# Kernel optimization log

Hardware: AMD Instinct MI355X
Metric: run time of the kernel (lower is better)

The kernel has to match this reference:

```python
import jax, jax.numpy as jnp
import numpy as np

N = 8192        # num nodes
D = 512         # hidden_dim
E = 262144      # num edges (avg degree 32)
STEPS = 3       # diffusion_steps


def setup_inputs() -> dict:
    key = jax.random.key(0)
    k1, k2, k3 = jax.random.split(key, 3)
    x = jax.random.normal(k1, (N, D), dtype=jnp.float32)
    edge_index = jax.random.randint(k2, (2, E), 0, N, dtype=jnp.int32)
    W = jax.random.normal(k3, (D, D), dtype=jnp.float32) / np.sqrt(D)
    b = jnp.zeros((D,), dtype=jnp.float32)
    diffusion_weights = jnp.ones((STEPS + 1,), dtype=jnp.float32) / (STEPS + 1)
    return {"x": x, "edge_index": edge_index, "W": W, "b": b,
            "diffusion_weights": diffusion_weights}


def reference(x, edge_index, W, b, diffusion_weights):
    # linear transform
    h = x @ W + b                                   # [N, D]
    # build symmetric normalized dense adjacency (faithful to original)
    row, col = edge_index[0], edge_index[1]
    adj = jnp.zeros((N, N), dtype=h.dtype)
    adj = adj.at[row, col].set(1.0)                 # adj[row, col] = 1
    adj = adj.at[col, row].set(1.0)                 # adj[col, row] = 1
    adj = adj + jnp.eye(N, dtype=h.dtype)           # self loops
    row_sum = adj.sum(axis=1, keepdims=True)
    adj = adj / jnp.maximum(row_sum, 1.0)           # row-normalize, clamp(min=1)
    # K-hop diffusion with learned per-hop weights
    out = diffusion_weights[0] * h
    cur = h
    for i in range(STEPS):
        cur = adj @ cur                             # [N, D]
        out = out + diffusion_weights[i + 1] * cur
    # relu; dropout is identity in eval mode
    return jax.nn.relu(out)
```

## Files before the change

kernel.cpp:

```cpp
#include <hip/hip_runtime.h>
#include <hip/hip_bf16.h>

#define NN 8192
#define DD 512
#define ROWWORDS (NN / 32)
#define MAXDEG 128
#define QCHUNK 256
#define SCL 8.0f

typedef __attribute__((ext_vector_type(8))) short short8;
typedef __attribute__((ext_vector_type(4))) float floatx4;
typedef __attribute__((ext_vector_type(2))) float f32x2;
typedef __attribute__((address_space(1))) const unsigned GASu;
typedef __attribute__((address_space(3))) unsigned LASu;

__device__ __forceinline__ unsigned short f2bf(float f) {
    union { float f; unsigned u; } v; v.f = f;
    unsigned u = v.u;
    return (unsigned short)((u + 0x7FFFu + ((u >> 16) & 1u)) >> 16);
}
__device__ __forceinline__ float bf2f(unsigned short s) {
    union { unsigned x; float f; } v; v.x = (unsigned)s << 16; return v.f;
}

__global__ __launch_bounds__(256) void prep_k(uint4* __restrict__ bm16,
                                              const float* __restrict__ x,
                                              unsigned short* __restrict__ xb,
                                              unsigned char* __restrict__ xq,
                                              const float* __restrict__ W,
                                              unsigned short* __restrict__ wbT,
                                              unsigned char* __restrict__ b1q,
                                              unsigned char* __restrict__ b2q) {
    const int j = blockIdx.x * 256 + threadIdx.x;
    bm16[j] = make_uint4(0u, 0u, 0u, 0u);
    const float4* xv = (const float4*)x;
    float4 v0 = xv[2 * j];
    float4 v1 = xv[2 * j + 1];
    ushort4 o0, o1;
    o0.x = f2bf(v0.x); o0.y = f2bf(v0.y); o0.z = f2bf(v0.z); o0.w = f2bf(v0.w);
    o1.x = f2bf(v1.x); o1.y = f2bf(v1.y); o1.z = f2bf(v1.z); o1.w = f2bf(v1.w);
    ((ushort4*)xb)[2 * j] = o0;
    ((ushort4*)xb)[2 * j + 1] = o1;
    unsigned qa = __builtin_amdgcn_cvt_pk_fp8_f32(SCL * v0.x, SCL * v0.y, 0, false);
    qa = __builtin_amdgcn_cvt_pk_fp8_f32(SCL * v0.z, SCL * v0.w, qa, true);
    unsigned qb = __builtin_amdgcn_cvt_pk_fp8_f32(SCL * v1.x, SCL * v1.y, 0, false);
    qb = __builtin_amdgcn_cvt_pk_fp8_f32(SCL * v1.z, SCL * v1.w, qb, true);
    ((uint2*)xq)[j] = make_uint2(qa, qb);
    if (j < DD * DD / 2) {
#pragma unroll
        for (int r = 0; r < 2; ++r) {
            int idx = j + r * (DD * DD / 2);
            int k = idx >> 9, c = idx & 511;
            wbT[(size_t)c * DD + k] = f2bf(W[idx]);
        }
    }
    if (blockIdx.x < 3 && threadIdx.x < 128) {
        unsigned char* pr = (blockIdx.x == 0 ? xq : blockIdx.x == 1 ? b1q : b2q)
                            + (size_t)NN * DD;
        ((unsigned*)pr)[threadIdx.x] = 0u;
    }
}

__global__ __launch_bounds__(256) void edges_k(const int* __restrict__ ei,
                                               unsigned* __restrict__ bm, int E) {
    int e = blockIdx.x * 256 + threadIdx.x;
    if (e >= E) return;
    int r = ei[e];
    int c = ei[E + e];
    atomicOr(&bm[(size_t)r * ROWWORDS + (c >> 5)], 1u << (c & 31));
    atomicOr(&bm[(size_t)c * ROWWORDS + (r >> 5)], 1u << (r & 31));
}

__global__ __launch_bounds__(256) void decode_k(const unsigned* __restrict__ bm,
                                                unsigned short* __restrict__ cols,
                                                int* __restrict__ deg) {
    const int i = blockIdx.x * 4 + (threadIdx.x >> 6);
    const int t = threadIdx.x & 63;
    const unsigned* rw = bm + (size_t)i * ROWWORDS + t * 4;
    unsigned w0 = rw[0], w1 = rw[1], w2 = rw[2], w3 = rw[3];
    int c = __popc(w0) + __popc(w1) + __popc(w2) + __popc(w3);
    int s = c;
    for (int d = 1; d < 64; d <<= 1) {
        int v = __shfl_up(s, d, 64);
        if (t >= d) s += v;
    }
    int p = s - c;
    const int n = __shfl(s, 63, 64);
    unsigned short* base = cols + (size_t)i * MAXDEG;
    const int cb = t * 128;
#pragma unroll
    for (int q = 0; q < 4; ++q) {
        unsigned w = (q == 0) ? w0 : (q == 1) ? w1 : (q == 2) ? w2 : w3;
        while (w) {
            int b = __ffs(w) - 1;
            w &= (w - 1);
            if (p < MAXDEG) base[p] = (unsigned short)(cb + q * 32 + b);
            ++p;
        }
    }
    if (t == 63) {
        int nc = (n < MAXDEG) ? n : MAXDEG;
        int npad = (nc + 15) & ~15;
        for (int q = nc; q < npad; ++q) base[q] = (unsigned short)NN;
        deg[i] = n;
    }
}

#define CVT(u, w) __builtin_amdgcn_cvt_pk_f32_fp8((int)(u), w)

#define ISSUE(P, js) do { \
    P##0 = *(const unsigned*)(cur + (size_t)(unsigned short)(js)[0] * DD + off); \
    P##1 = *(const unsigned*)(cur + (size_t)(unsigned short)(js)[1] * DD + off); \
    P##2 = *(const unsigned*)(cur + (size_t)(unsigned short)(js)[2] * DD + off); \
    P##3 = *(const unsigned*)(cur + (size_t)(unsigned short)(js)[3] * DD + off); \
    P##4 = *(const unsigned*)(cur + (size_t)(unsigned short)(js)[4] * DD + off); \
    P##5 = *(const unsigned*)(cur + (size_t)(unsigned short)(js)[5] * DD + off); \
    P##6 = *(const unsigned*)(cur + (size_t)(unsigned short)(js)[6] * DD + off); \
    P##7 = *(const unsigned*)(cur + (size_t)(unsigned short)(js)[7] * DD + off); \
} while (0)

#define CONSUME(P) do { \
    lA += CVT(P##0, false); hA += CVT(P##0, true); \
    lB += CVT(P##1, false); hB += CVT(P##1, true); \
    lA += CVT(P##2, false); hA += CVT(P##2, true); \
    lB += CVT(P##3, false); hB += CVT(P##3, true); \
    lA += CVT(P##4, false); hA += CVT(P##4, true); \
    lB += CVT(P##5, false); hB += CVT(P##5, true); \
    lA += CVT(P##6, false); hA += CVT(P##6, true); \
    lB += CVT(P##7, false); hB += CVT(P##7, true); \
} while (0)

__global__ __launch_bounds__(64, 8) void spmm_k(const unsigned char* __restrict__ cur,
                                             unsigned char* __restrict__ nxt,
                                             const unsigned short* __restrict__ cols,
                                             const int* __restrict__ deg,
                                             const float* __restrict__ dw,
                                             const unsigned short* __restrict__ xb,
                                             const unsigned char* __restrict__ b1q,
                                             const unsigned char* __restrict__ b2q,
                                             unsigned short* __restrict__ yb,
                                             int last) {
    const int bid = blockIdx.x;
    const int chunk = bid & 1;
    const int i = bid >> 1;
    const int t = threadIdx.x;
    const int off = chunk * QCHUNK + 4 * t;
    const size_t rowb = (size_t)i * DD;
    const int n = deg[i];
    const int nc = (n < MAXDEG) ? n : MAXDEG;
    const int nb = ((nc + 15) & ~15) >> 3;
    const unsigned short* cl = cols + (size_t)i * MAXDEG;

    const unsigned eu = *(const unsigned*)(cur + rowb + off);

    f32x2 lA = {0.f, 0.f}, hA = lA, lB = lA, hB = lA;
    if (nb) {
        unsigned cA0, cA1, cA2, cA3, cA4, cA5, cA6, cA7;
        unsigned cB0, cB1, cB2, cB3, cB4, cB5, cB6, cB7;
        short8 jsA = *(const short8*)(cl);
        ISSUE(cA, jsA);
        short8 jsB = *(const short8*)(cl + 8);
        ISSUE(cB, jsB);
        for (int b = 2; b < nb; b += 2) {
            short8 jsC = *(const short8*)(cl + (size_t)b * 8);
            short8 jsD = *(const short8*)(cl + (size_t)b * 8 + 8);
            CONSUME(cA);
            ISSUE(cA, jsC);
            CONSUME(cB);
            ISSUE(cB, jsD);
        }
        CONSUME(cA);
        CONSUME(cB);
    }
    f32x2 lo = lA + lB;
    f32x2 hi = hA + hB;
    lo += CVT(eu, false);
    hi += CVT(eu, true);
    const float inv = 1.0f / (float)(n + 1);
    lo *= inv; hi *= inv;

    if (!last) {
        unsigned o = __builtin_amdgcn_cvt_pk_fp8_f32(lo.x, lo.y, 0, false);
        o = __builtin_amdgcn_cvt_pk_fp8_f32(hi.x, hi.y, o, true);
        *(unsigned*)(nxt + rowb + off) = o;
    } else {
        const float w0 = dw[0];
        const float s1 = dw[1] * (1.0f / SCL);
        const float s2 = dw[2] * (1.0f / SCL);
        const float s3 = dw[3] * (1.0f / SCL);
        ushort4 xv = *(const ushort4*)(xb + rowb + off);
        unsigned u1 = *(const unsigned*)(b1q + rowb + off);
        unsigned u2 = *(const unsigned*)(b2q + rowb + off);
        f32x2 b1l = CVT(u1, false), b1h = CVT(u1, true);
        f32x2 b2l = CVT(u2, false), b2h = CVT(u2, true);
        float y0 = w0 * bf2f(xv.x) + s1 * b1l.x + s2 * b2l.x + s3 * lo.x;
        float y1 = w0 * bf2f(xv.y) + s1 * b1l.y + s2 * b2l.y + s3 * lo.y;
        float y2 = w0 * bf2f(xv.z) + s1 * b1h.x + s2 * b2h.x + s3 * hi.x;
        float y3 = w0 * bf2f(xv.w) + s1 * b1h.y + s2 * b2h.y + s3 * hi.y;
        ushort4 o;
        o.x = f2bf(y0); o.y = f2bf(y1); o.z = f2bf(y2); o.w = f2bf(y3);
        *(ushort4*)(yb + rowb + off) = o;
    }
}

__global__ __launch_bounds__(256) void gemm_k(const unsigned short* __restrict__ yb,
                                              const unsigned short* __restrict__ wbT,
                                              const float* __restrict__ bias,
                                              const float* __restrict__ dw, int nw,
                                              float* __restrict__ out) {
    __shared__ unsigned short Asm[128 * 64];
    __shared__ unsigned short Bsm[128 * 64];
    const int t = threadIdx.x;
    const int l = t & 63;
    const int wid = t >> 6;
    const int wm = wid >> 1, wn = wid & 1;
    const int row0 = blockIdx.x * 128;
    const int col0 = blockIdx.y * 128;
    const int lr = l & 15;

    floatx4 acc[4][4];
#pragma unroll
    for (int a = 0; a < 4; ++a)
#pragma unroll
        for (int b = 0; b < 4; ++b) acc[a][b] = (floatx4){0.f, 0.f, 0.f, 0.f};

    for (int k0 = 0; k0 < DD; k0 += 64) {
#pragma unroll
        for (int p = 0; p < 4; ++p) {
            int e = p * 256 + t;
            int r = e >> 3;
            int sl = e & 7;
            int gs = (sl ^ (r & 7)) * 8;
            __builtin_amdgcn_global_load_lds(
                (GASu*)(yb + (size_t)(row0 + r) * DD + k0 + gs),
                (LASu*)(Asm + (size_t)e * 8), 16, 0, 0);
            __builtin_amdgcn_global_load_lds(
                (GASu*)(wbT + (size_t)(col0 + r) * DD + k0 + gs),
                (LASu*)(Bsm + (size_t)e * 8), 16, 0, 0);
        }
        __syncthreads();
#pragma unroll
        for (int ks = 0; ks < 2; ++ks) {
            short8 af[4], bf[4];
#pragma unroll
            for (int mt = 0; mt < 4; ++mt) {
                int R = wm * 64 + mt * 16 + lr;
                int sl = (l >> 4) + 4 * ks;
                af[mt] = *(const short8*)(Asm + R * 64 + (sl ^ (R & 7)) * 8);
            }
#pragma unroll
            for (int nt = 0; nt < 4; ++nt) {
                int R = wn * 64 + nt * 16 + lr;
                int sl = (l >> 4) + 4 * ks;
                bf[nt] = *(const short8*)(Bsm + R * 64 + (sl ^ (R & 7)) * 8);
            }
#pragma unroll
            for (int mt = 0; mt < 4; ++mt)
#pragma unroll
                for (int nt = 0; nt < 4; ++nt)
                    acc[mt][nt] = __builtin_amdgcn_mfma_f32_16x16x32_bf16(
                        af[mt], bf[nt], acc[mt][nt], 0, 0, 0);
        }
        __syncthreads();
    }

    float sb = 0.f;
    for (int q = 0; q < nw; ++q) sb += dw[q];
#pragma unroll
    for (int nt = 0; nt < 4; ++nt) {
        int col = col0 + wn * 64 + nt * 16 + lr;
        float bv = bias[col] * sb;
#pragma unroll
        for (int mt = 0; mt < 4; ++mt) {
            int rowb = row0 + wm * 64 + mt * 16 + (l >> 4) * 4;
#pragma unroll
            for (int r = 0; r < 4; ++r) {
                float v = acc[mt][nt][r] + bv;
                v = fmaxf(v, 0.0f);
                out[(size_t)(rowb + r) * DD + col] = v;
            }
        }
    }
}

extern "C" void kernel_launch(void* const* d_in, const int* in_sizes, int n_in,
                              void* d_out, int out_size, void* d_ws, size_t ws_size,
                              hipStream_t stream) {
    const float* x    = (const float*)d_in[0];
    const int*   ei   = (const int*)d_in[1];
    const float* W    = (const float*)d_in[2];
    const float* bias = (const float*)d_in[3];
    const float* dw   = (const float*)d_in[4];
    const int E = in_sizes[1] / 2;
    const int nw = in_sizes[4];

    char* outc = (char*)d_out;
    unsigned* bitmap     = (unsigned*)outc;
    unsigned short* cols = (unsigned short*)(outc + (size_t)8 * 1024 * 1024);
    int* deg             = (int*)(outc + (size_t)12 * 1024 * 1024);

    const size_t MB = 1024 * 1024;
    char* ws = (char*)d_ws;
    unsigned short* xb  = (unsigned short*)(ws);
    unsigned short* yb  = (unsigned short*)(ws + 8 * MB);
    unsigned short* wbT = (unsigned short*)(ws + 16 * MB);
    unsigned char*  xq  = (unsigned char*)(ws + 17 * MB);
    unsigned char*  b1q = (unsigned char*)(ws + 22 * MB);
    unsigned char*  b2q = (unsigned char*)(ws + 27 * MB);

    prep_k<<<2048, 256, 0, stream>>>((uint4*)bitmap, x, xb, xq, W, wbT, b1q, b2q);
    edges_k<<<(E + 255) / 256, 256, 0, stream>>>(ei, bitmap, E);
    decode_k<<<NN / 4, 256, 0, stream>>>(bitmap, cols, deg);

    spmm_k<<<NN * 2, 64, 0, stream>>>(xq,  b1q, cols, deg, dw, xb, b1q, b2q, yb, 0);
    spmm_k<<<NN * 2, 64, 0, stream>>>(b1q, b2q, cols, deg, dw, xb, b1q, b2q, yb, 0);
    spmm_k<<<NN * 2, 64, 0, stream>>>(b2q, b1q, cols, deg, dw, xb, b1q, b2q, yb, 1);

    gemm_k<<<dim3(NN / 128, DD / 128), 256, 0, stream>>>(yb, wbT, bias, dw, nw,
                                                         (float*)d_out);
}
```

Measured before the change: 104.1 us.

## Build neighbor lists directly in edge kernel, dropping bitmap decode pass

The edge kernel now uses the return value of atomicOr to detect first insertion of each edge. It then appends the neighbor to a per-row column list through an atomicAdd counter. This removes the separate decode kernel, which re-read the whole 8 MB bitmap and scanned bits per row, along with one launch. The prep kernel pre-fills the column lists with the padding index NN and zeroes the counters. Neighbor order becomes non-deterministic, so summation order varies between runs, and the counter atomics add some contention.

```diff
diff --git a/kernel.cpp b/kernel.cpp
--- a/kernel.cpp
+++ b/kernel.cpp
@@ -29,10 +29,14 @@
                                               unsigned char* __restrict__ xq,
                                               const float* __restrict__ W,
                                               unsigned short* __restrict__ wbT,
+                                              unsigned* __restrict__ cols32,
+                                              int* __restrict__ cnt,
                                               unsigned char* __restrict__ b1q,
                                               unsigned char* __restrict__ b2q) {
     const int j = blockIdx.x * 256 + threadIdx.x;
     bm16[j] = make_uint4(0u, 0u, 0u, 0u);
+    cols32[j] = 0x20002000u;
+    if (j < NN / 4) ((int4*)cnt)[j] = make_int4(0, 0, 0, 0);
     const float4* xv = (const float4*)x;
     float4 v0 = xv[2 * j];
     float4 v1 = xv[2 * j + 1];
@@ -62,47 +66,24 @@
 }
 
 __global__ __launch_bounds__(256) void edges_k(const int* __restrict__ ei,
-                                               unsigned* __restrict__ bm, int E) {
+                                               unsigned* __restrict__ bm,
+                                               unsigned short* __restrict__ cols,
+                                               int* __restrict__ cnt, int E) {
     int e = blockIdx.x * 256 + threadIdx.x;
     if (e >= E) return;
     int r = ei[e];
     int c = ei[E + e];
-    atomicOr(&bm[(size_t)r * ROWWORDS + (c >> 5)], 1u << (c & 31));
-    atomicOr(&bm[(size_t)c * ROWWORDS + (r >> 5)], 1u << (r & 31));
-}
-
-__global__ __launch_bounds__(256) void decode_k(const unsigned* __restrict__ bm,
-                                                unsigned short* __restrict__ cols,
-                                                int* __restrict__ deg) {
-    const int i = blockIdx.x * 4 + (threadIdx.x >> 6);
-    const int t = threadIdx.x & 63;
-    const unsigned* rw = bm + (size_t)i * ROWWORDS + t * 4;
-    unsigned w0 = rw[0], w1 = rw[1], w2 = rw[2], w3 = rw[3];
-    int c = __popc(w0) + __popc(w1) + __popc(w2) + __popc(w3);
-    int s = c;
-    for (int d = 1; d < 64; d <<= 1) {
-        int v = __shfl_up(s, d, 64);
-        if (t >= d) s += v;
-    }
-    int p = s - c;
-    const int n = __shfl(s, 63, 64);
-    unsigned short* base = cols + (size_t)i * MAXDEG;
-    const int cb = t * 128;
-#pragma unroll
-    for (int q = 0; q < 4; ++q) {
-        unsigned w = (q == 0) ? w0 : (q == 1) ? w1 : (q == 2) ? w2 : w3;
-        while (w) {
-            int b = __ffs(w) - 1;
-            w &= (w - 1);
-            if (p < MAXDEG) base[p] = (unsigned short)(cb + q * 32 + b);
-            ++p;
-        }
-    }
-    if (t == 63) {
-        int nc = (n < MAXDEG) ? n : MAXDEG;
-        int npad = (nc + 15) & ~15;
-        for (int q = nc; q < npad; ++q) base[q] = (unsigned short)NN;
-        deg[i] = n;
+    unsigned m = 1u << (c & 31);
+    unsigned old = atomicOr(&bm[(size_t)r * ROWWORDS + (c >> 5)], m);
+    if (!(old & m)) {
+        int p = atomicAdd(&cnt[r], 1);
+        if (p < MAXDEG) cols[(size_t)r * MAXDEG + p] = (unsigned short)c;
+    }
+    m = 1u << (r & 31);
+    old = atomicOr(&bm[(size_t)c * ROWWORDS + (r >> 5)], m);
+    if (!(old & m)) {
+        int p = atomicAdd(&cnt[c], 1);
+        if (p < MAXDEG) cols[(size_t)c * MAXDEG + p] = (unsigned short)r;
     }
 }
 
@@ -297,7 +278,7 @@
     char* outc = (char*)d_out;
     unsigned* bitmap     = (unsigned*)outc;
     unsigned short* cols = (unsigned short*)(outc + (size_t)8 * 1024 * 1024);
-    int* deg             = (int*)(outc + (size_t)12 * 1024 * 1024);
+    int* cnt             = (int*)(outc + (size_t)10 * 1024 * 1024);
 
     const size_t MB = 1024 * 1024;
     char* ws = (char*)d_ws;
@@ -308,13 +289,13 @@
     unsigned char*  b1q = (unsigned char*)(ws + 22 * MB);
     unsigned char*  b2q = (unsigned char*)(ws + 27 * MB);
 
-    prep_k<<<2048, 256, 0, stream>>>((uint4*)bitmap, x, xb, xq, W, wbT, b1q, b2q);
-    edges_k<<<(E + 255) / 256, 256, 0, stream>>>(ei, bitmap, E);
-    decode_k<<<NN / 4, 256, 0, stream>>>(bitmap, cols, deg);
-
-    spmm_k<<<NN * 2, 64, 0, stream>>>(xq,  b1q, cols, deg, dw, xb, b1q, b2q, yb, 0);
-    spmm_k<<<NN * 2, 64, 0, stream>>>(b1q, b2q, cols, deg, dw, xb, b1q, b2q, yb, 0);
-    spmm_k<<<NN * 2, 64, 0, stream>>>(b2q, b1q, cols, deg, dw, xb, b1q, b2q, yb, 1);
+    prep_k<<<2048, 256, 0, stream>>>((uint4*)bitmap, x, xb, xq, W, wbT,
+                                     (unsigned*)cols, cnt, b1q, b2q);
+    edges_k<<<(E + 255) / 256, 256, 0, stream>>>(ei, bitmap, cols, cnt, E);
+
+    spmm_k<<<NN * 2, 64, 0, stream>>>(xq,  b1q, cols, cnt, dw, xb, b1q, b2q, yb, 0);
+    spmm_k<<<NN * 2, 64, 0, stream>>>(b1q, b2q, cols, cnt, dw, xb, b1q, b2q, yb, 0);
+    spmm_k<<<NN * 2, 64, 0, stream>>>(b2q, b1q, cols, cnt, dw, xb, b1q, b2q, yb, 1);
 
     gemm_k<<<dim3(NN / 128, DD / 128), 256, 0, stream>>>(yb, wbT, bias, dw, nw,
                                                          (float*)d_out);
```

Measured after the change: 121.6 us. 1.17x slower.
